# Optimization experiments

Hardware: AMD Instinct MI355X
Metric: run time of the kernel (lower is better)

Reference implementation:

```python
import jax, jax.numpy as jnp
import numpy as np

NUM_HEADS = 16

def setup_inputs() -> dict:
    key = jax.random.key(0)
    k1, k2, k3 = jax.random.split(key, 3)
    B, S, D = 4, 2048, 1024
    x = jax.random.normal(k1, (B, S, D), dtype=jnp.float32)
    # xavier-uniform-like small init so unscaled logits stay numerically sane
    w_qkv = jax.random.normal(k2, (3 * D, D), dtype=jnp.float32) * 0.02
    w_out = jax.random.normal(k3, (D, D), dtype=jnp.float32) * 0.02
    return {"x": x, "w_qkv": w_qkv, "w_out": w_out}

def reference(x, w_qkv, w_out):
    B, S, D = x.shape
    H = NUM_HEADS
    d = D // H
    # qkv projection (Linear, no bias): x @ W^T -> [B, S, 3D]
    qkv = jnp.einsum('bsd,ed->bse', x, w_qkv).reshape(B, S, H, 3 * d)
    q, k, v = jnp.split(qkv, 3, axis=-1)           # each [B, S, H, d]
    q = q.transpose(0, 2, 1, 3)                    # [B, H, S, d]
    k = k.transpose(0, 2, 1, 3)
    v = v.transpose(0, 2, 1, 3)
    # NOTE: the original module does NOT scale by 1/sqrt(d) — faithful.
    logits = jnp.einsum('bhqd,bhkd->bhqk', q, k)   # [B, H, S, S]
    attn = jax.nn.softmax(logits, axis=-1)
    vals = jnp.einsum('bhqk,bhkd->bhqd', attn, v)  # [B, H, S, d]
    vals = vals.transpose(0, 2, 1, 3).reshape(B, S, D)
    return jnp.einsum('bsd,od->bso', vals, w_out)
```

## Files before the change

kernel.cpp:

```cpp
#include <hip/hip_runtime.h>
#include <hip/hip_bf16.h>

#define DEVINL __device__ __forceinline__

typedef short bf16x4 __attribute__((ext_vector_type(4)));
typedef short bf16x8 __attribute__((ext_vector_type(8)));
typedef float f32x4 __attribute__((ext_vector_type(4)));
typedef float f32x16 __attribute__((ext_vector_type(16)));
typedef unsigned short us4 __attribute__((ext_vector_type(4)));


DEVINL unsigned short f2bf(float f) {
  unsigned u = __builtin_bit_cast(unsigned, f);
  unsigned r = u + 0x7fffu + ((u >> 16) & 1u);
  return (unsigned short)(r >> 16);
}

DEVINL f32x4 mfma32(bf16x8 a, bf16x8 b, f32x4 c) {
  return __builtin_amdgcn_mfma_f32_16x16x32_bf16(a, b, c, 0, 0, 0);
}

DEVINL f32x16 mfma3216(bf16x8 a, bf16x8 b, f32x16 c) {
  return __builtin_amdgcn_mfma_f32_32x32x16_bf16(a, b, c, 0, 0, 0);
}

DEVINL float fexp2(float x) {
#if __has_builtin(__builtin_amdgcn_exp2f)
  return __builtin_amdgcn_exp2f(x);
#else
  return exp2f(x);
#endif
}

DEVINL unsigned cvt_pk_bf16(float a, float b) {
  unsigned r;
  asm("v_cvt_pk_bf16_f32 %0, %1, %2" : "=v"(r) : "v"(a), "v"(b));
  return r;
}

DEVINL void permswap(unsigned& x, unsigned& y) {
#if __has_builtin(__builtin_amdgcn_permlane32_swap)
  typedef int i32x2_t __attribute__((ext_vector_type(2)));
  i32x2_t r = __builtin_amdgcn_permlane32_swap((int)x, (int)y, false, false);
  x = (unsigned)r[0];
  y = (unsigned)r[1];
#else
  asm("v_permlane32_swap_b32 %0, %1" : "+v"(x), "+v"(y));
#endif
}

#define GLOAD_LDS16(g, l)                                                    \
  __builtin_amdgcn_global_load_lds(                                          \
      (__attribute__((address_space(1))) void*)(unsigned short*)(g),         \
      (__attribute__((address_space(3))) void*)(l), 16, 0, 0)

__global__ void cvtk(const float* __restrict__ src,
                     unsigned short* __restrict__ dst, int n4) {
  int i = blockIdx.x * 256 + threadIdx.x;
  const int st = gridDim.x * 256;
  for (; i < n4; i += st) {
    const float4 v = ((const float4*)src)[i];
    us4 o;
    o[0] = f2bf(v.x); o[1] = f2bf(v.y); o[2] = f2bf(v.z); o[3] = f2bf(v.w);
    ((us4*)dst)[i] = o;
  }
}

__global__ __launch_bounds__(256, 2) void qkv_gemm(
    const unsigned short* __restrict__ A,
    const unsigned short* __restrict__ Bw,
    unsigned short* __restrict__ Qo,
    unsigned short* __restrict__ Ko,
    unsigned short* __restrict__ VTo) {
  constexpr int K = 1024, BK = 32;
  __shared__ unsigned short As[128 * BK];
  __shared__ unsigned short Bs[128 * BK];
  const int tid = threadIdx.x;
  const int lane = tid & 63;
  const int wid = tid >> 6;
  const int l15 = lane & 15, g = lane >> 4;
  const int fid = blockIdx.y * 24 + blockIdx.x;
  const int swzid = (fid & 7) * 192 + (fid >> 3);
  const int m0 = (swzid / 24) * 128;
  const int n0 = (swzid % 24) * 128;
  const int wr = wid >> 1, wc = wid & 1;

  f32x4 acc[4][4] = {};

  const int sidx0 = tid * 8;
  const int sidx1 = (256 + tid) * 8;
  const int r0 = sidx0 >> 5, c0 = sidx0 & 31;
  const int r1 = sidx1 >> 5, c1 = sidx1 & 31;

  for (int k0 = 0; k0 < K; k0 += BK) {
    __syncthreads();
    GLOAD_LDS16(A + (size_t)(m0 + r0) * K + k0 + c0, As + sidx0);
    GLOAD_LDS16(Bw + (size_t)(n0 + r0) * K + k0 + c0, Bs + sidx0);
    GLOAD_LDS16(A + (size_t)(m0 + r1) * K + k0 + c1, As + sidx1);
    GLOAD_LDS16(Bw + (size_t)(n0 + r1) * K + k0 + c1, Bs + sidx1);
    __syncthreads();
    bf16x8 af[4], bfr[4];
#pragma unroll
    for (int i = 0; i < 4; ++i) {
      af[i] = *(const bf16x8*)(As + (wr * 64 + i * 16 + l15) * BK + g * 8);
      bfr[i] = *(const bf16x8*)(Bs + (wc * 64 + i * 16 + l15) * BK + g * 8);
    }
#pragma unroll
    for (int mi = 0; mi < 4; ++mi)
#pragma unroll
      for (int ni = 0; ni < 4; ++ni)
        acc[mi][ni] = mfma32(af[mi], bfr[ni], acc[mi][ni]);
  }

#pragma unroll
  for (int mi = 0; mi < 4; ++mi) {
    const int mbase = m0 + wr * 64 + mi * 16 + g * 4;
#pragma unroll
    for (int ni = 0; ni < 4; ++ni) {
      const int e = n0 + wc * 64 + ni * 16 + l15;
      const int h = e / 192;
      const int r = e - h * 192;
#pragma unroll
      for (int j = 0; j < 4; ++j) {
        const int mm = mbase + j;
        const int b = mm >> 11, s = mm & 2047;
        const int bh = b * 16 + h;
        if (r < 64)
          Qo[((size_t)bh * 2048 + s) * 64 + r] =
              f2bf(acc[mi][ni][j] * 1.44269504f);
        else if (r < 128)
          Ko[((size_t)bh * 2048 + s) * 64 + (r - 64)] = f2bf(acc[mi][ni][j]);
        else
          VTo[((size_t)bh * 64 + (r - 128)) * 2048 + s] = f2bf(acc[mi][ni][j]);
      }
    }
  }
}

__global__ __launch_bounds__(256, 2) void attn_fwd(
    const unsigned short* __restrict__ Q,
    const unsigned short* __restrict__ K,
    const unsigned short* __restrict__ VT,
    unsigned short* __restrict__ Vals) {
  __shared__ unsigned short Ks[2][128 * 64];
  __shared__ unsigned short Vs[2][64 * 128];
  __shared__ float invs[4][2][32];
  const int tid = threadIdx.x;
  const int lane = tid & 63;
  const int wid = tid >> 6;
  const int l31 = lane & 31;
  const int hi = lane >> 5;
  const int bid = (blockIdx.x & 7) * 64 + (blockIdx.x >> 3);
  const int bh = bid >> 3;
  const int q0 = (bid & 7) * 256 + wid * 64;
  const unsigned short* Qb = Q + (size_t)bh * (2048 * 64);
  const unsigned short* Kb = K + (size_t)bh * (2048 * 64);
  const unsigned short* Vb = VT + (size_t)bh * (64 * 2048);

  bf16x8 qf[2][4];
#pragma unroll
  for (int qt = 0; qt < 2; ++qt) {
    const unsigned short* qrow = Qb + (size_t)(q0 + qt * 32 + l31) * 64;
#pragma unroll
    for (int kw = 0; kw < 4; ++kw)
      qf[qt][kw] = *(const bf16x8*)(qrow + kw * 16 + hi * 8);
  }

  float lsum[2] = {0.0f, 0.0f};
  f32x16 o[2][2] = {};
  const unsigned swz = (unsigned)((l31 & 7) << 4);
  const unsigned laneK = (unsigned)(l31 * 128) + (((unsigned)hi << 4) ^ swz);
  const unsigned laneV = (unsigned)(l31 * 256) + (((unsigned)hi << 4) ^ swz);

#define STAGE(kv0, nb)                                                       \
  {                                                                          \
    _Pragma("unroll") for (int j = 0; j < 4; ++j) {                          \
      const int c = tid + j * 256;                                           \
      const int kr = c >> 3;                                                 \
      const int ksc = ((((c & 7) << 4) ^ ((kr & 7) << 4)) >> 1);             \
      GLOAD_LDS16(Kb + (size_t)((kv0) + kr) * 64 + ksc, &Ks[nb][c * 8]);     \
      const int vr = c >> 4;                                                 \
      const int vsc = ((((c & 15) << 4) ^ ((vr & 7) << 4)) >> 1);            \
      GLOAD_LDS16(Vb + (size_t)vr * 2048 + (kv0) + vsc, &Vs[nb][c * 8]);     \
    }                                                                        \
  }

  STAGE(0, 0);
  __syncthreads();

  for (int kv0 = 0; kv0 < 2048; kv0 += 128) {
    const int cur = (kv0 >> 7) & 1;
    if (kv0 + 128 < 2048) STAGE(kv0 + 128, cur ^ 1);
    const char* kb = (const char*)Ks[cur];
    const char* vb = (const char*)Vs[cur];
#pragma unroll
    for (int sub = 0; sub < 4; ++sub) {
      const unsigned kbase = laneK + (unsigned)(sub * 4096);
      bf16x8 kf[4];
#pragma unroll
      for (int kw = 0; kw < 4; ++kw)
        kf[kw] = *(const bf16x8*)(kb + (kbase ^ (unsigned)(kw * 32)));
      f32x16 s0 = {}, s1 = {};
      __builtin_amdgcn_s_setprio(1);
#pragma unroll
      for (int kw = 0; kw < 4; ++kw) s0 = mfma3216(kf[kw], qf[0][kw], s0);
#pragma unroll
      for (int kw = 0; kw < 4; ++kw) s1 = mfma3216(kf[kw], qf[1][kw], s1);
      __builtin_amdgcn_s_setprio(0);
#pragma unroll
      for (int half = 0; half < 2; ++half) {
        const int pb = half * 8;
        const unsigned ksoff = (unsigned)((sub * 2 + half) * 32);
        const bf16x8 vf0 = *(const bf16x8*)(vb + (laneV ^ ksoff));
        const bf16x8 vf1 = *(const bf16x8*)(vb + ((laneV + 8192u) ^ ksoff));
#pragma unroll
        for (int qt = 0; qt < 2; ++qt) {
          const f32x16& s = qt ? s1 : s0;
          const float p0 = fexp2(s[pb + 0]);
          const float p1 = fexp2(s[pb + 1]);
          const float p2 = fexp2(s[pb + 2]);
          const float p3 = fexp2(s[pb + 3]);
          const float p4 = fexp2(s[pb + 4]);
          const float p5 = fexp2(s[pb + 5]);
          const float p6 = fexp2(s[pb + 6]);
          const float p7 = fexp2(s[pb + 7]);
          lsum[qt] += ((p0 + p1) + (p2 + p3)) + ((p4 + p5) + (p6 + p7));
          unsigned w0 = cvt_pk_bf16(p0, p1);
          unsigned w2 = cvt_pk_bf16(p4, p5);
          permswap(w0, w2);
          unsigned w1 = cvt_pk_bf16(p2, p3);
          unsigned w3 = cvt_pk_bf16(p6, p7);
          permswap(w1, w3);
          union {
            unsigned u[4];
            bf16x8 v;
          } pk;
          pk.u[0] = w0;
          pk.u[1] = w1;
          pk.u[2] = w2;
          pk.u[3] = w3;
          __builtin_amdgcn_s_setprio(1);
          o[qt][0] = mfma3216(pk.v, vf0, o[qt][0]);
          o[qt][1] = mfma3216(pk.v, vf1, o[qt][1]);
          __builtin_amdgcn_s_setprio(0);
        }
      }
    }
    __syncthreads();
  }
#undef STAGE

#pragma unroll
  for (int qt = 0; qt < 2; ++qt) {
    const float ltot = lsum[qt] + __shfl_xor(lsum[qt], 32);
    invs[wid][qt][l31] = 1.0f / ltot;
  }
  const int b = bh >> 4, h = bh & 15;
#pragma unroll
  for (int qt = 0; qt < 2; ++qt) {
    unsigned short* ob =
        Vals + (size_t)(b * 2048 + q0 + qt * 32) * 1024 + h * 64 + l31;
#pragma unroll
    for (int j = 0; j < 16; ++j) {
      const int ql = (j & 3) + 8 * (j >> 2) + 4 * hi;
      const float inv = invs[wid][qt][ql];
      ob[(size_t)ql * 1024] = f2bf(o[qt][0][j] * inv);
      ob[(size_t)ql * 1024 + 32] = f2bf(o[qt][1][j] * inv);
    }
  }
}

__global__ __launch_bounds__(256, 2) void out_gemm(
    const unsigned short* __restrict__ A,
    const unsigned short* __restrict__ Bw,
    float* __restrict__ C) {
  constexpr int K = 1024, BK = 32;
  __shared__ unsigned short As[128 * BK];
  __shared__ unsigned short Bs[128 * BK];
  const int tid = threadIdx.x;
  const int lane = tid & 63;
  const int wid = tid >> 6;
  const int l15 = lane & 15, g = lane >> 4;
  const int fid = blockIdx.y * 8 + blockIdx.x;
  const int swzid = (fid & 7) * 64 + (fid >> 3);
  const int m0 = (swzid >> 3) * 128;
  const int n0 = (swzid & 7) * 128;
  const int wr = wid >> 1, wc = wid & 1;

  f32x4 acc[4][4] = {};

  const int sidx0 = tid * 8;
  const int sidx1 = (256 + tid) * 8;
  const int r0 = sidx0 >> 5, c0 = sidx0 & 31;
  const int r1 = sidx1 >> 5, c1 = sidx1 & 31;

  for (int k0 = 0; k0 < K; k0 += BK) {
    __syncthreads();
    GLOAD_LDS16(A + (size_t)(m0 + r0) * K + k0 + c0, As + sidx0);
    GLOAD_LDS16(Bw + (size_t)(n0 + r0) * K + k0 + c0, Bs + sidx0);
    GLOAD_LDS16(A + (size_t)(m0 + r1) * K + k0 + c1, As + sidx1);
    GLOAD_LDS16(Bw + (size_t)(n0 + r1) * K + k0 + c1, Bs + sidx1);
    __syncthreads();
    bf16x8 af[4], bfr[4];
#pragma unroll
    for (int i = 0; i < 4; ++i) {
      af[i] = *(const bf16x8*)(As + (wr * 64 + i * 16 + l15) * BK + g * 8);
      bfr[i] = *(const bf16x8*)(Bs + (wc * 64 + i * 16 + l15) * BK + g * 8);
    }
#pragma unroll
    for (int mi = 0; mi < 4; ++mi)
#pragma unroll
      for (int ni = 0; ni < 4; ++ni)
        acc[mi][ni] = mfma32(af[mi], bfr[ni], acc[mi][ni]);
  }

#pragma unroll
  for (int mi = 0; mi < 4; ++mi) {
    const int mbase = m0 + wr * 64 + mi * 16 + g * 4;
#pragma unroll
    for (int ni = 0; ni < 4; ++ni) {
      const int n = n0 + wc * 64 + ni * 16 + l15;
#pragma unroll
      for (int j = 0; j < 4; ++j)
        C[(size_t)(mbase + j) * 1024 + n] = acc[mi][ni][j];
    }
  }
}

extern "C" void kernel_launch(void* const* d_in, const int* in_sizes, int n_in,
                              void* d_out, int out_size, void* d_ws,
                              size_t ws_size, hipStream_t stream) {
  const float* x = (const float*)d_in[0];
  const float* w_qkv = (const float*)d_in[1];
  const float* w_out = (const float*)d_in[2];
  float* out = (float*)d_out;

  char* ws = (char*)d_ws;
  unsigned short* xb = (unsigned short*)(ws);
  unsigned short* wqkvb = (unsigned short*)(ws + (16u << 20));
  unsigned short* woutb = (unsigned short*)(ws + (22u << 20));
  unsigned short* Qt = (unsigned short*)(ws + (24u << 20));
  unsigned short* Kt = (unsigned short*)(ws + (40u << 20));
  unsigned short* VTt = (unsigned short*)(ws + (56u << 20));
  unsigned short* vals = xb;

  cvtk<<<2048, 256, 0, stream>>>(x, xb, 8388608 / 4);
  cvtk<<<2048, 256, 0, stream>>>(w_qkv, wqkvb, 3145728 / 4);
  cvtk<<<1024, 256, 0, stream>>>(w_out, woutb, 1048576 / 4);
  qkv_gemm<<<dim3(24, 64), 256, 0, stream>>>(xb, wqkvb, Qt, Kt, VTt);
  attn_fwd<<<512, 256, 0, stream>>>(Qt, Kt, VTt, vals);
  out_gemm<<<dim3(8, 64), 256, 0, stream>>>(vals, woutb, out);
}
```

Before: 194.8 us.

## Rewrite projection GEMMs with 256x128 tiles, double-buffered async LDS pipeline

```diff
diff --git a/kernel.cpp b/kernel.cpp
--- a/kernel.cpp
+++ b/kernel.cpp
@@ -14,10 +14,6 @@
   unsigned u = __builtin_bit_cast(unsigned, f);
   unsigned r = u + 0x7fffu + ((u >> 16) & 1u);
   return (unsigned short)(r >> 16);
-}
-
-DEVINL f32x4 mfma32(bf16x8 a, bf16x8 b, f32x4 c) {
-  return __builtin_amdgcn_mfma_f32_16x16x32_bf16(a, b, c, 0, 0, 0);
 }
 
 DEVINL f32x16 mfma3216(bf16x8 a, bf16x8 b, f32x16 c) {
@@ -54,6 +50,9 @@
       (__attribute__((address_space(1))) void*)(unsigned short*)(g),         \
       (__attribute__((address_space(3))) void*)(l), 16, 0, 0)
 
+#define VMCNT(n) asm volatile("s_waitcnt vmcnt(" #n ")" ::: "memory")
+#define SBARRIER asm volatile("s_barrier" ::: "memory")
+
 __global__ void cvtk(const float* __restrict__ src,
                      unsigned short* __restrict__ dst, int n4) {
   int i = blockIdx.x * 256 + threadIdx.x;
@@ -66,64 +65,101 @@
   }
 }
 
-__global__ __launch_bounds__(256, 2) void qkv_gemm(
+#define GEMM_BODY(Ab, Bb)                                                    \
+  const int tid = threadIdx.x;                                               \
+  const int lane = tid & 63;                                                 \
+  const int wid = tid >> 6;                                                  \
+  const int l31 = lane & 31, hi = lane >> 5;                                 \
+  const int wm = wid >> 1, wn = wid & 1;                                     \
+  const int ca0 = tid, ca1 = tid + 512;                                      \
+  const int ra0 = ca0 >> 2, ra1 = ca1 >> 2;                                  \
+  const int sa0 = (((ca0 & 3) ^ (ra0 & 3)) * 8);                             \
+  const int sa1 = (((ca1 & 3) ^ (ra1 & 3)) * 8);                             \
+  const int da0 = ca0 * 8, da1 = ca1 * 8;                                    \
+  const int rb0 = tid >> 2;                                                  \
+  const int sb0 = (((tid & 3) ^ (rb0 & 3)) * 8);                             \
+  const int db0 = tid * 8;                                                   \
+  f32x16 acc[2][2] = {};                                                     \
+       \
+  STGA(0, 0); STGB(0, 0);                                                    \
+  STGA(0, 1); STGB(0, 1);                                                    \
+  STGA(1, 0); STGB(1, 0);                                                    \
+  VMCNT(6);                                                                  \
+  SBARRIER;                                                                  \
+  for (int t = 0; t < 16; ++t) {                                             \
+    const int dbf = t & 1;                                                   \
+    _Pragma("unroll") for (int ph = 0; ph < 2; ++ph) {                       \
+      bf16x8 af[2][2], bfr[2][2];                                            \
+      _Pragma("unroll") for (int ksl = 0; ksl < 2; ++ksl) {                  \
+        _Pragma("unroll") for (int mi = 0; mi < 2; ++mi) {                   \
+          const int r = wm * 64 + mi * 32 + l31;                             \
+          const int off = ((ksl * 32 + hi * 16) ^ ((r & 3) << 4)) >> 1;      \
+          af[ksl][mi] = *(const bf16x8*)&Al[dbf][ph][r * 32 + off];          \
+        }                                                                    \
+        _Pragma("unroll") for (int ni = 0; ni < 2; ++ni) {                   \
+          const int r = wn * 64 + ni * 32 + l31;                             \
+          const int off = ((ksl * 32 + hi * 16) ^ ((r & 3) << 4)) >> 1;      \
+          bfr[ksl][ni] = *(const bf16x8*)&Bl[dbf][ph][r * 32 + off];         \
+        }                                                                    \
+      }                                                                      \
+      if (ph == 0) {                                                         \
+        if (t < 15) { STGA(t + 1, 1); STGB(t + 1, 1); }                      \
+        if (t < 15) { VMCNT(6); } else { VMCNT(0); }                         \
+      } else {                                                               \
+        if (t < 14) { STGA(t + 2, 0); STGB(t + 2, 0); }                      \
+        if (t < 14) { VMCNT(6); }                                            \
+        else if (t == 14) { VMCNT(3); }                                      \
+        else { VMCNT(0); }                                                   \
+      }                                                                      \
+      SBARRIER;                                                              \
+      __builtin_amdgcn_s_setprio(1);                                         \
+      _Pragma("unroll") for (int ksl = 0; ksl < 2; ++ksl)                    \
+      _Pragma("unroll") for (int mi = 0; mi < 2; ++mi)                       \
+      _Pragma("unroll") for (int ni = 0; ni < 2; ++ni)                       \
+          acc[mi][ni] = mfma3216(af[ksl][mi], bfr[ksl][ni], acc[mi][ni]);    \
+      __builtin_amdgcn_s_setprio(0);                                         \
+    }                                                                        \
+  }
+
+#define STGA(ts, kh_)                                                        \
+  {                                                                          \
+    const int kb = (ts) * 64 + (kh_) * 32;                                   \
+    GLOAD_LDS16(Ab + (size_t)ra0 * 1024 + kb + sa0, &Al[(ts) & 1][kh_][da0]);\
+    GLOAD_LDS16(Ab + (size_t)ra1 * 1024 + kb + sa1, &Al[(ts) & 1][kh_][da1]);\
+  }
+#define STGB(ts, kh_)                                                        \
+  {                                                                          \
+    const int kb = (ts) * 64 + (kh_) * 32;                                   \
+    GLOAD_LDS16(Bb + (size_t)rb0 * 1024 + kb + sb0, &Bl[(ts) & 1][kh_][db0]);\
+  }
+
+__global__ __launch_bounds__(512, 2) void qkv_gemm(
     const unsigned short* __restrict__ A,
     const unsigned short* __restrict__ Bw,
     unsigned short* __restrict__ Qo,
     unsigned short* __restrict__ Ko,
     unsigned short* __restrict__ VTo) {
-  constexpr int K = 1024, BK = 32;
-  __shared__ unsigned short As[128 * BK];
-  __shared__ unsigned short Bs[128 * BK];
-  const int tid = threadIdx.x;
-  const int lane = tid & 63;
-  const int wid = tid >> 6;
-  const int l15 = lane & 15, g = lane >> 4;
-  const int fid = blockIdx.y * 24 + blockIdx.x;
-  const int swzid = (fid & 7) * 192 + (fid >> 3);
-  const int m0 = (swzid / 24) * 128;
-  const int n0 = (swzid % 24) * 128;
-  const int wr = wid >> 1, wc = wid & 1;
-
-  f32x4 acc[4][4] = {};
-
-  const int sidx0 = tid * 8;
-  const int sidx1 = (256 + tid) * 8;
-  const int r0 = sidx0 >> 5, c0 = sidx0 & 31;
-  const int r1 = sidx1 >> 5, c1 = sidx1 & 31;
-
-  for (int k0 = 0; k0 < K; k0 += BK) {
-    __syncthreads();
-    GLOAD_LDS16(A + (size_t)(m0 + r0) * K + k0 + c0, As + sidx0);
-    GLOAD_LDS16(Bw + (size_t)(n0 + r0) * K + k0 + c0, Bs + sidx0);
-    GLOAD_LDS16(A + (size_t)(m0 + r1) * K + k0 + c1, As + sidx1);
-    GLOAD_LDS16(Bw + (size_t)(n0 + r1) * K + k0 + c1, Bs + sidx1);
-    __syncthreads();
-    bf16x8 af[4], bfr[4];
-#pragma unroll
-    for (int i = 0; i < 4; ++i) {
-      af[i] = *(const bf16x8*)(As + (wr * 64 + i * 16 + l15) * BK + g * 8);
-      bfr[i] = *(const bf16x8*)(Bs + (wc * 64 + i * 16 + l15) * BK + g * 8);
-    }
-#pragma unroll
-    for (int mi = 0; mi < 4; ++mi)
-#pragma unroll
-      for (int ni = 0; ni < 4; ++ni)
-        acc[mi][ni] = mfma32(af[mi], bfr[ni], acc[mi][ni]);
-  }
-
-#pragma unroll
-  for (int mi = 0; mi < 4; ++mi) {
-    const int mbase = m0 + wr * 64 + mi * 16 + g * 4;
-#pragma unroll
-    for (int ni = 0; ni < 4; ++ni) {
-      const int e = n0 + wc * 64 + ni * 16 + l15;
+  __shared__ unsigned short Al[2][2][256 * 32];
+  __shared__ unsigned short Bl[2][2][128 * 32];
+  const int swzid = (blockIdx.x & 7) * 96 + (blockIdx.x >> 3);
+  const int mt = swzid / 24, nt = swzid % 24;
+  const unsigned short* Ab = A + (size_t)mt * 256 * 1024;
+  const unsigned short* Bb = Bw + (size_t)nt * 128 * 1024;
+
+  GEMM_BODY(Ab, Bb)
+
+#pragma unroll
+  for (int mi = 0; mi < 2; ++mi) {
+#pragma unroll
+    for (int ni = 0; ni < 2; ++ni) {
+      const int e = nt * 128 + wn * 64 + ni * 32 + l31;
       const int h = e / 192;
       const int r = e - h * 192;
 #pragma unroll
-      for (int j = 0; j < 4; ++j) {
-        const int mm = mbase + j;
-        const int b = mm >> 11, s = mm & 2047;
+      for (int j = 0; j < 16; ++j) {
+        const int crow = (j & 3) + 8 * (j >> 2) + 4 * hi;
+        const int m = mt * 256 + wm * 64 + mi * 32 + crow;
+        const int b = m >> 11, s = m & 2047;
         const int bh = b * 16 + h;
         if (r < 64)
           Qo[((size_t)bh * 2048 + s) * 64 + r] =
@@ -132,6 +168,34 @@
           Ko[((size_t)bh * 2048 + s) * 64 + (r - 64)] = f2bf(acc[mi][ni][j]);
         else
           VTo[((size_t)bh * 64 + (r - 128)) * 2048 + s] = f2bf(acc[mi][ni][j]);
+      }
+    }
+  }
+}
+
+__global__ __launch_bounds__(512, 2) void out_gemm(
+    const unsigned short* __restrict__ A,
+    const unsigned short* __restrict__ Bw,
+    float* __restrict__ C) {
+  __shared__ unsigned short Al[2][2][256 * 32];
+  __shared__ unsigned short Bl[2][2][128 * 32];
+  const int swzid = (blockIdx.x & 7) * 32 + (blockIdx.x >> 3);
+  const int mt = swzid >> 3, nt = swzid & 7;
+  const unsigned short* Ab = A + (size_t)mt * 256 * 1024;
+  const unsigned short* Bb = Bw + (size_t)nt * 128 * 1024;
+
+  GEMM_BODY(Ab, Bb)
+
+#pragma unroll
+  for (int mi = 0; mi < 2; ++mi) {
+#pragma unroll
+    for (int ni = 0; ni < 2; ++ni) {
+      const int n = nt * 128 + wn * 64 + ni * 32 + l31;
+#pragma unroll
+      for (int j = 0; j < 16; ++j) {
+        const int crow = (j & 3) + 8 * (j >> 2) + 4 * hi;
+        const int m = mt * 256 + wm * 64 + mi * 32 + crow;
+        C[(size_t)m * 1024 + n] = acc[mi][ni][j];
       }
     }
   }
@@ -270,63 +334,6 @@
   }
 }
 
-__global__ __launch_bounds__(256, 2) void out_gemm(
-    const unsigned short* __restrict__ A,
-    const unsigned short* __restrict__ Bw,
-    float* __restrict__ C) {
-  constexpr int K = 1024, BK = 32;
-  __shared__ unsigned short As[128 * BK];
-  __shared__ unsigned short Bs[128 * BK];
-  const int tid = threadIdx.x;
-  const int lane = tid & 63;
-  const int wid = tid >> 6;
-  const int l15 = lane & 15, g = lane >> 4;
-  const int fid = blockIdx.y * 8 + blockIdx.x;
-  const int swzid = (fid & 7) * 64 + (fid >> 3);
-  const int m0 = (swzid >> 3) * 128;
-  const int n0 = (swzid & 7) * 128;
-  const int wr = wid >> 1, wc = wid & 1;
-
-  f32x4 acc[4][4] = {};
-
-  const int sidx0 = tid * 8;
-  const int sidx1 = (256 + tid) * 8;
-  const int r0 = sidx0 >> 5, c0 = sidx0 & 31;
-  const int r1 = sidx1 >> 5, c1 = sidx1 & 31;
-
-  for (int k0 = 0; k0 < K; k0 += BK) {
-    __syncthreads();
-    GLOAD_LDS16(A + (size_t)(m0 + r0) * K + k0 + c0, As + sidx0);
-    GLOAD_LDS16(Bw + (size_t)(n0 + r0) * K + k0 + c0, Bs + sidx0);
-    GLOAD_LDS16(A + (size_t)(m0 + r1) * K + k0 + c1, As + sidx1);
-    GLOAD_LDS16(Bw + (size_t)(n0 + r1) * K + k0 + c1, Bs + sidx1);
-    __syncthreads();
-    bf16x8 af[4], bfr[4];
-#pragma unroll
-    for (int i = 0; i < 4; ++i) {
-      af[i] = *(const bf16x8*)(As + (wr * 64 + i * 16 + l15) * BK + g * 8);
-      bfr[i] = *(const bf16x8*)(Bs + (wc * 64 + i * 16 + l15) * BK + g * 8);
-    }
-#pragma unroll
-    for (int mi = 0; mi < 4; ++mi)
-#pragma unroll
-      for (int ni = 0; ni < 4; ++ni)
-        acc[mi][ni] = mfma32(af[mi], bfr[ni], acc[mi][ni]);
-  }
-
-#pragma unroll
-  for (int mi = 0; mi < 4; ++mi) {
-    const int mbase = m0 + wr * 64 + mi * 16 + g * 4;
-#pragma unroll
-    for (int ni = 0; ni < 4; ++ni) {
-      const int n = n0 + wc * 64 + ni * 16 + l15;
-#pragma unroll
-      for (int j = 0; j < 4; ++j)
-        C[(size_t)(mbase + j) * 1024 + n] = acc[mi][ni][j];
-    }
-  }
-}
-
 extern "C" void kernel_launch(void* const* d_in, const int* in_sizes, int n_in,
                               void* d_out, int out_size, void* d_ws,
                               size_t ws_size, hipStream_t stream) {
@@ -347,7 +354,7 @@
   cvtk<<<2048, 256, 0, stream>>>(x, xb, 8388608 / 4);
   cvtk<<<2048, 256, 0, stream>>>(w_qkv, wqkvb, 3145728 / 4);
   cvtk<<<1024, 256, 0, stream>>>(w_out, woutb, 1048576 / 4);
-  qkv_gemm<<<dim3(24, 64), 256, 0, stream>>>(xb, wqkvb, Qt, Kt, VTt);
+  qkv_gemm<<<768, 512, 0, stream>>>(xb, wqkvb, Qt, Kt, VTt);
   attn_fwd<<<512, 256, 0, stream>>>(Qt, Kt, VTt, vals);
-  out_gemm<<<dim3(8, 64), 256, 0, stream>>>(vals, woutb, out);
-}
+  out_gemm<<<256, 512, 0, stream>>>(vals, woutb, out);
+}
```

Result: slower. 207.5 us (+6.5%).

## Double-buffer QKV GEMM LDS loads and vectorize epilogue stores via LDS staging

Applied to the files above, without the earlier changes.

```diff
diff --git a/kernel.cpp b/kernel.cpp
--- a/kernel.cpp
+++ b/kernel.cpp
@@ -72,9 +72,8 @@
     unsigned short* __restrict__ Qo,
     unsigned short* __restrict__ Ko,
     unsigned short* __restrict__ VTo) {
-  constexpr int K = 1024, BK = 32;
-  __shared__ unsigned short As[128 * BK];
-  __shared__ unsigned short Bs[128 * BK];
+  constexpr int K = 1024;
+  __shared__ unsigned short SH[16384];
   const int tid = threadIdx.x;
   const int lane = tid & 63;
   const int wid = tid >> 6;
@@ -92,47 +91,86 @@
   const int r0 = sidx0 >> 5, c0 = sidx0 & 31;
   const int r1 = sidx1 >> 5, c1 = sidx1 & 31;
 
-  for (int k0 = 0; k0 < K; k0 += BK) {
-    __syncthreads();
-    GLOAD_LDS16(A + (size_t)(m0 + r0) * K + k0 + c0, As + sidx0);
-    GLOAD_LDS16(Bw + (size_t)(n0 + r0) * K + k0 + c0, Bs + sidx0);
-    GLOAD_LDS16(A + (size_t)(m0 + r1) * K + k0 + c1, As + sidx1);
-    GLOAD_LDS16(Bw + (size_t)(n0 + r1) * K + k0 + c1, Bs + sidx1);
-    __syncthreads();
+#define QSTAGE(kt, bb)                                                       \
+  {                                                                          \
+    const int k0_ = (kt)*32;                                                 \
+    GLOAD_LDS16(A + (size_t)(m0 + r0) * K + k0_ + c0,                        \
+                SH + (bb)*8192 + sidx0);                                     \
+    GLOAD_LDS16(Bw + (size_t)(n0 + r0) * K + k0_ + c0,                       \
+                SH + (bb)*8192 + 4096 + sidx0);                              \
+    GLOAD_LDS16(A + (size_t)(m0 + r1) * K + k0_ + c1,                        \
+                SH + (bb)*8192 + sidx1);                                     \
+    GLOAD_LDS16(Bw + (size_t)(n0 + r1) * K + k0_ + c1,                       \
+                SH + (bb)*8192 + 4096 + sidx1);                              \
+  }
+
+  QSTAGE(0, 0);
+  __syncthreads();
+
+  for (int t = 0; t < 32; ++t) {
+    const int cb = t & 1;
+    if (t < 31) QSTAGE(t + 1, cb ^ 1);
     bf16x8 af[4], bfr[4];
 #pragma unroll
     for (int i = 0; i < 4; ++i) {
-      af[i] = *(const bf16x8*)(As + (wr * 64 + i * 16 + l15) * BK + g * 8);
-      bfr[i] = *(const bf16x8*)(Bs + (wc * 64 + i * 16 + l15) * BK + g * 8);
+      af[i] =
+          *(const bf16x8*)(SH + cb * 8192 + (wr * 64 + i * 16 + l15) * 32 +
+                           g * 8);
+      bfr[i] = *(const bf16x8*)(SH + cb * 8192 + 4096 +
+                                (wc * 64 + i * 16 + l15) * 32 + g * 8);
     }
 #pragma unroll
     for (int mi = 0; mi < 4; ++mi)
 #pragma unroll
       for (int ni = 0; ni < 4; ++ni)
         acc[mi][ni] = mfma32(af[mi], bfr[ni], acc[mi][ni]);
-  }
-
-#pragma unroll
-  for (int mi = 0; mi < 4; ++mi) {
-    const int mbase = m0 + wr * 64 + mi * 16 + g * 4;
-#pragma unroll
-    for (int ni = 0; ni < 4; ++ni) {
-      const int e = n0 + wc * 64 + ni * 16 + l15;
-      const int h = e / 192;
-      const int r = e - h * 192;
-#pragma unroll
-      for (int j = 0; j < 4; ++j) {
-        const int mm = mbase + j;
-        const int b = mm >> 11, s = mm & 2047;
+    __syncthreads();
+  }
+#undef QSTAGE
+
+#pragma unroll
+  for (int ni = 0; ni < 4; ++ni) {
+    const int ebase = n0 + wc * 64 + ni * 16;
+    const int h = ebase / 192;
+    const int rbase = ebase - h * 192;
+#pragma unroll
+    for (int mi = 0; mi < 4; ++mi) {
+      const int mbase = m0 + wr * 64 + mi * 16 + g * 4;
+      if (rbase >= 128) {
+        const int rv = rbase + l15 - 128;
+        const int b = mbase >> 11, s = mbase & 2047;
         const int bh = b * 16 + h;
-        if (r < 64)
-          Qo[((size_t)bh * 2048 + s) * 64 + r] =
-              f2bf(acc[mi][ni][j] * 1.44269504f);
-        else if (r < 128)
-          Ko[((size_t)bh * 2048 + s) * 64 + (r - 64)] = f2bf(acc[mi][ni][j]);
-        else
-          VTo[((size_t)bh * 64 + (r - 128)) * 2048 + s] = f2bf(acc[mi][ni][j]);
+        us4 ov;
+#pragma unroll
+        for (int j = 0; j < 4; ++j) ov[j] = f2bf(acc[mi][ni][j]);
+        *(us4*)(VTo + ((size_t)bh * 64 + rv) * 2048 + s) = ov;
+      } else {
+        const float scale = (rbase < 64) ? 1.44269504f : 1.0f;
+        const int eloc = wc * 64 + ni * 16 + l15;
+        const int mloc = wr * 64 + mi * 16 + g * 4;
+#pragma unroll
+        for (int j = 0; j < 4; ++j)
+          SH[(mloc + j) * 128 + eloc] = f2bf(acc[mi][ni][j] * scale);
       }
+    }
+  }
+  __syncthreads();
+#pragma unroll
+  for (int k = 0; k < 8; ++k) {
+    const int c = tid + k * 256;
+    const int ml = c >> 4, e8 = (c & 15) * 8;
+    const int e0 = n0 + e8;
+    const int h = e0 / 192;
+    const int r = e0 - h * 192;
+    if (r < 128) {
+      const int mm = m0 + ml;
+      const int b = mm >> 11, s = mm & 2047;
+      const int bh = b * 16 + h;
+      const bf16x8 v = *(const bf16x8*)&SH[ml * 128 + e8];
+      if (r < 64)
+        *(bf16x8*)(Qo + ((size_t)bh * 2048 + s) * 64 + r) = v;
+      else
+        *(bf16x8*)(Ko + ((size_t)bh * 2048 + s) * 64 + (r - 64)) = v;
     }
   }
 }
```

Measured after the change: 186.5 us. -4.3%, faster.
